# Kernel tuning notes

Hardware: AMD Instinct MI355X
Metric: run time of the kernel (lower is better)

The kernel has to match this reference:

```python
import jax, jax.numpy as jnp
import numpy as np

N_NODES = 100000
N_EDGES = 1600000
IN_CH = 128
HID = 128
OUT_CH = 64
N_GRAPHS = 512


def gcn_conv(x, edge_index, W, b):
    # GCNConv (PyG defaults): add self-loops, symmetric normalization
    # out = D^{-1/2} (A + I) D^{-1/2} X W + b
    n = x.shape[0]
    loop = jnp.arange(n, dtype=edge_index.dtype)
    src = jnp.concatenate([edge_index[0], loop])
    dst = jnp.concatenate([edge_index[1], loop])
    deg = jax.ops.segment_sum(jnp.ones_like(dst, x.dtype), dst, num_segments=n)
    dinv = jnp.where(deg > 0, jax.lax.rsqrt(deg), jnp.zeros_like(deg))
    norm = dinv[src] * dinv[dst]            # [E+N]
    h = x @ W                                # [N, out] transform first (dense GEMM)
    msg = h[src] * norm[:, None]             # gather + scale  [E+N, out]
    return jax.ops.segment_sum(msg, dst, num_segments=n) + b


def global_mean_pool(x, batch, num_graphs):
    sums = jax.ops.segment_sum(x, batch, num_segments=num_graphs)
    cnts = jax.ops.segment_sum(jnp.ones_like(batch, x.dtype), batch, num_segments=num_graphs)
    return sums / jnp.maximum(cnts, 1.0)[:, None]


def setup_inputs() -> dict:
    key = jax.random.key(0)
    ks = jax.random.split(key, 12)
    x = jax.random.normal(ks[0], (N_NODES, IN_CH), dtype=jnp.float32)
    edge_index = jax.random.randint(ks[1], (2, N_EDGES), 0, N_NODES, dtype=jnp.int64)
    batch = jnp.sort(jax.random.randint(ks[2], (N_NODES,), 0, N_GRAPHS, dtype=jnp.int64))
    def glorot(k, fi, fo):
        s = float(np.sqrt(6.0 / (fi + fo)))
        return jax.random.uniform(k, (fi, fo), jnp.float32, -s, s)
    W1 = glorot(ks[3], IN_CH, HID); b1 = jnp.zeros((HID,), jnp.float32)
    W2 = glorot(ks[4], HID, HID);   b2 = jnp.zeros((HID,), jnp.float32)
    W3 = glorot(ks[5], HID, HID);   b3 = jnp.zeros((HID,), jnp.float32)
    W4 = glorot(ks[6], HID, OUT_CH); b4 = jnp.zeros((OUT_CH,), jnp.float32)
    return {"x": x, "edge_index": edge_index, "batch": batch,
            "W1": W1, "b1": b1, "W2": W2, "b2": b2,
            "W3": W3, "b3": b3, "W4": W4, "b4": b4}


def reference(x, edge_index, batch, W1, b1, W2, b2, W3, b3, W4, b4):
    h = jax.nn.relu(gcn_conv(x, edge_index, W1, b1))
    h = jax.nn.relu(gcn_conv(h, edge_index, W2, b2))
    g = global_mean_pool(h, batch, N_GRAPHS)           # [G, HID]
    # MLP head; Dropout(0.2) is identity in eval mode
    g = jax.nn.relu(g @ W3 + b3)
    return g @ W4 + b4                                  # [G, OUT_CH]
```

## Files before the change

### kernel.cpp

```cpp
#include <hip/hip_runtime.h>

#define NN 100000
#define EE 1600000
#define CH 128
#define NG 512
#define OC 64

#define CSH 10
#define NCB 98
#define PBLK 256
#define PCHUNK 6250
#define SCAP 128

#define O_DINV   0
#define O_ROWS   200128
#define O_CNT    300160
#define O_PART   400192
#define O_OFFS   400320
#define O_CSR    400448
#define O_HS     2000448
#define O_STG    8400448
#define O_WT1    8400448
#define O_WT2    8416832
#define O_A1     14800448
#define O_START  27600448

typedef __attribute__((ext_vector_type(8))) short short8v;
typedef __attribute__((ext_vector_type(4))) float float4v;

static __device__ __forceinline__ unsigned short f2bf(float x) {
  unsigned u = __float_as_uint(x);
  return (unsigned short)((u + 0x7FFFu + ((u >> 16) & 1u)) >> 16);
}
static __device__ __forceinline__ float bf2f(unsigned short h) {
  return __uint_as_float((unsigned)h << 16);
}
static __device__ __forceinline__ float bflo(unsigned v) {
  return __uint_as_float(v << 16);
}
static __device__ __forceinline__ float bfhi(unsigned v) {
  return __uint_as_float(v & 0xFFFF0000u);
}

__global__ __launch_bounds__(1024) void k_part(const int* __restrict__ src,
                                               const int* __restrict__ dst,
                                               int* __restrict__ cnt,
                                               unsigned* __restrict__ stg) {
  __shared__ int hist[NCB];
  __shared__ int lcur[NCB];
  __shared__ unsigned lout[PCHUNK];
  int t = threadIdx.x;
  int e0 = blockIdx.x * PCHUNK;
  if (t < NCB) { hist[t] = 0; lcur[t] = 0; }
  __syncthreads();
  for (int e = e0 + t; e < e0 + PCHUNK; e += 1024)
    atomicAdd(&hist[dst[e] >> CSH], 1);
  __syncthreads();
  if (t == 0) {
    int s = 0;
    for (int i = 0; i < NCB; ++i) { int v = hist[i]; hist[i] = s; s += v; }
  }
  __syncthreads();
  for (int e = e0 + t; e < e0 + PCHUNK; e += 1024) {
    int d = dst[e];
    int b = d >> CSH;
    int p = hist[b] + atomicAdd(&lcur[b], 1);
    lout[p] = (unsigned)src[e] | ((unsigned)(d & 1023) << 17);
  }
  __syncthreads();
  int w = t >> 6, lane = t & 63;
  unsigned* mystg = stg + (size_t)blockIdx.x * NCB * SCAP;
  for (int b = w; b < NCB; b += 16) {
    int beg = hist[b];
    int end = (b == NCB - 1) ? PCHUNK : hist[b + 1];
    int n = min(end - beg, SCAP);
    for (int i = lane; i < n; i += 64) mystg[b * SCAP + i] = lout[beg + i];
    if (lane == 0) cnt[blockIdx.x * NCB + b] = n;
  }
}

__global__ __launch_bounds__(1024) void k_count(const unsigned* __restrict__ stg,
                                                const int* __restrict__ cnt,
                                                int* __restrict__ rows,
                                                int* __restrict__ part,
                                                float* __restrict__ dinv) {
  __shared__ int ldeg[1024];
  __shared__ int s[1024];
  int b = blockIdx.x;
  int t = threadIdx.x;
  int w = t >> 6, lane = t & 63;
  int gid = (b << CSH) + t;
  ldeg[t] = 0;
  __syncthreads();
  for (int blk = w; blk < PBLK; blk += 16) {
    int c = cnt[blk * NCB + b];
    const unsigned* p = stg + ((size_t)blk * NCB + b) * SCAP;
    for (int e = lane; e < c; e += 64) atomicAdd(&ldeg[p[e] >> 17], 1);
  }
  __syncthreads();
  int v = ldeg[t];
  if (gid < NN) dinv[gid] = rsqrtf((float)(v + 1));
  s[t] = v;
  __syncthreads();
  for (int off = 1; off < 1024; off <<= 1) {
    int u = (t >= off) ? s[t - off] : 0;
    __syncthreads();
    if (t >= off) s[t] += u;
    __syncthreads();
  }
  if (gid < NN) rows[gid] = s[t] - v;
  if (t == 1023) part[b] = s[t];
}

__global__ void k_scan_part(const int* __restrict__ part, int* __restrict__ offs) {
  __shared__ int s[128];
  int t = threadIdx.x;
  int v = (t < NCB) ? part[t] : 0;
  s[t] = v;
  __syncthreads();
  for (int off = 1; off < 128; off <<= 1) {
    int u = (t >= off) ? s[t - off] : 0;
    __syncthreads();
    if (t >= off) s[t] += u;
    __syncthreads();
  }
  if (t < NCB) offs[t] = s[t] - v;
}

__global__ void k_scan_add(int* __restrict__ rows, const int* __restrict__ offs,
                           const int* __restrict__ batch, int* __restrict__ start) {
  int i = blockIdx.x * 256 + threadIdx.x;
  if (i >= NN) return;
  rows[i] += offs[i >> 10];
  if (i == 0) rows[NN] = EE;
  int b = batch[i];
  int prev = (i == 0) ? -1 : batch[i - 1];
  for (int g = prev + 1; g <= b; ++g) start[g] = i;
  if (i == NN - 1)
    for (int g = b + 1; g <= NG; ++g) start[g] = NN;
}

__global__ __launch_bounds__(1024) void k_place(const unsigned* __restrict__ stg,
                                                const int* __restrict__ cnt,
                                                const int* __restrict__ rows,
                                                int* __restrict__ csr) {
  __shared__ int lrow[1024];
  __shared__ int lcur[1024];
  int b = blockIdx.x;
  int t = threadIdx.x;
  int w = t >> 6, lane = t & 63;
  int gid = (b << CSH) + t;
  lrow[t] = (gid < NN) ? rows[gid] : 0;
  lcur[t] = 0;
  __syncthreads();
  for (int blk = w; blk < PBLK; blk += 16) {
    int c = cnt[blk * NCB + b];
    const unsigned* p = stg + ((size_t)blk * NCB + b) * SCAP;
    for (int e = lane; e < c; e += 64) {
      unsigned x = p[e];
      int ld = x >> 17;
      int q = atomicAdd(&lcur[ld], 1);
      csr[lrow[ld] + q] = (int)(x & 0x1FFFFu);
    }
  }
}

__global__ void k_wsplit(const float* __restrict__ W1, const float* __restrict__ W2,
                         unsigned short* __restrict__ wt1,
                         unsigned short* __restrict__ wt2) {
  int id = blockIdx.x * 256 + threadIdx.x;
  const float* W = (id < 16384) ? W1 : W2;
  unsigned short* wt = (id < 16384) ? wt1 : wt2;
  int i = id & 16383;
  int k = i >> 7, n = i & 127;
  float w = W[i];
  unsigned short h = f2bf(w);
  unsigned short l = f2bf(w - bf2f(h));
  wt[n * 128 + k] = h;
  wt[16384 + n * 128 + k] = l;
}

__global__ __launch_bounds__(256) void k_gemm_mfma(
    const float* __restrict__ X, const unsigned short* __restrict__ wth,
    const unsigned short* __restrict__ wtl, const float* __restrict__ dinv,
    unsigned short* __restrict__ Hs) {
  __shared__ __align__(16) unsigned short sWh[64 * 136];
  __shared__ __align__(16) unsigned short sWl[64 * 136];
  __shared__ __align__(16) unsigned short sXh[128 * 40];
  __shared__ __align__(16) unsigned short sXl[128 * 40];

  const int t = threadIdx.x;
  const int w = t >> 6, lane = t & 63;
  const int quad = lane >> 4, lr = lane & 15;
  const int row0 = blockIdx.x * 128;
  const int col0 = blockIdx.y * 64;

#pragma unroll
  for (int j = 0; j < 8; ++j) {
    int id = t + j * 256;
    int n = id >> 5, kk = (id & 31) * 4;
    *(ushort4*)&sWh[n * 136 + kk] = *(const ushort4*)&wth[(col0 + n) * 128 + kk];
    *(ushort4*)&sWl[n * 136 + kk] = *(const ushort4*)&wtl[(col0 + n) * 128 + kk];
  }

  float4v acc[2][4];
#pragma unroll
  for (int mi = 0; mi < 2; ++mi)
#pragma unroll
    for (int ni = 0; ni < 4; ++ni) acc[mi][ni] = (float4v){0.f, 0.f, 0.f, 0.f};

  for (int ks = 0; ks < 4; ++ks) {
    const int k0 = ks * 32;
    if (ks) __syncthreads();
#pragma unroll
    for (int i = 0; i < 4; ++i) {
      int row = i * 32 + (t >> 3);
      int seg = t & 7;
      int gr = row0 + row;
      float4 xv = {0.f, 0.f, 0.f, 0.f};
      if (gr < NN) xv = *(const float4*)&X[(size_t)gr * CH + k0 + seg * 4];
      ushort4 h, l;
      h.x = f2bf(xv.x); l.x = f2bf(xv.x - bf2f(h.x));
      h.y = f2bf(xv.y); l.y = f2bf(xv.y - bf2f(h.y));
      h.z = f2bf(xv.z); l.z = f2bf(xv.z - bf2f(h.z));
      h.w = f2bf(xv.w); l.w = f2bf(xv.w - bf2f(h.w));
      *(ushort4*)&sXh[row * 40 + seg * 4] = h;
      *(ushort4*)&sXl[row * 40 + seg * 4] = l;
    }
    __syncthreads();

    short8v ah[2], al[2];
#pragma unroll
    for (int mi = 0; mi < 2; ++mi) {
      int r = w * 32 + mi * 16 + lr;
      ah[mi] = *(const short8v*)&sXh[r * 40 + quad * 8];
      al[mi] = *(const short8v*)&sXl[r * 40 + quad * 8];
    }
#pragma unroll
    for (int ni = 0; ni < 4; ++ni) {
      int n = ni * 16 + lr;
      short8v bh = *(const short8v*)&sWh[n * 136 + k0 + quad * 8];
      short8v bl = *(const short8v*)&sWl[n * 136 + k0 + quad * 8];
#pragma unroll
      for (int mi = 0; mi < 2; ++mi) {
        acc[mi][ni] = __builtin_amdgcn_mfma_f32_16x16x32_bf16(ah[mi], bh, acc[mi][ni], 0, 0, 0);
        acc[mi][ni] = __builtin_amdgcn_mfma_f32_16x16x32_bf16(ah[mi], bl, acc[mi][ni], 0, 0, 0);
        acc[mi][ni] = __builtin_amdgcn_mfma_f32_16x16x32_bf16(al[mi], bh, acc[mi][ni], 0, 0, 0);
      }
    }
  }

#pragma unroll
  for (int mi = 0; mi < 2; ++mi) {
#pragma unroll
    for (int r = 0; r < 4; ++r) {
      int grow = row0 + w * 32 + mi * 16 + quad * 4 + r;
      if (grow < NN) {
        float d = dinv[grow];
#pragma unroll
        for (int ni = 0; ni < 4; ++ni)
          Hs[(size_t)grow * CH + col0 + ni * 16 + lr] = f2bf(d * acc[mi][ni][r]);
      }
    }
  }
}

__global__ __launch_bounds__(256) void k_aggregate(
    const unsigned* __restrict__ H, const int* __restrict__ rows,
    const int* __restrict__ csr, const float* __restrict__ dinv,
    const float* __restrict__ bias, float* __restrict__ out) {
  int node = blockIdx.x * 4 + (threadIdx.x >> 6);
  int lane = threadIdx.x & 63;
  if (node >= NN) return;
  float bx = bias[2 * lane], by = bias[2 * lane + 1];
  unsigned sv = H[(size_t)node * 64 + lane];
  float ax = bflo(sv), ay = bfhi(sv);
  int e0 = rows[node], e1 = rows[node + 1];
  int deg = e1 - e0;
  if (deg > 0) {
    int elast = e1 - 1;
    unsigned va[8], vb[8];
#pragma unroll
    for (int k = 0; k < 8; ++k) {
      int ee = e0 + k;
      int j = csr[ee <= elast ? ee : elast];
      va[k] = H[(size_t)j * 64 + lane];
    }
    int ngroups = (deg + 7) >> 3;
    int base = e0;
    for (int g = 1; g < ngroups; ++g) {
      int nb = e0 + g * 8;
#pragma unroll
      for (int k = 0; k < 8; ++k) {
        int ee = nb + k;
        int j = csr[ee <= elast ? ee : elast];
        vb[k] = H[(size_t)j * 64 + lane];
      }
#pragma unroll
      for (int k = 0; k < 8; ++k) { ax += bflo(va[k]); ay += bfhi(va[k]); }
#pragma unroll
      for (int k = 0; k < 8; ++k) va[k] = vb[k];
      base = nb;
    }
    int rem = e1 - base;
#pragma unroll
    for (int k = 0; k < 8; ++k) {
      unsigned v = (k < rem) ? va[k] : 0u;
      ax += bflo(v);
      ay += bfhi(v);
    }
  }
  float d = dinv[node];
  float2 o;
  o.x = fmaxf(fmaf(d, ax, bx), 0.f);
  o.y = fmaxf(fmaf(d, ay, by), 0.f);
  ((float2*)out)[(size_t)node * 64 + lane] = o;
}

__global__ __launch_bounds__(256) void k_head(
    const float* __restrict__ A, const int* __restrict__ start,
    const float* __restrict__ W3, const float* __restrict__ b3,
    const float* __restrict__ W4, const float* __restrict__ b4,
    float* __restrict__ out) {
  __shared__ float pooled[128];
  __shared__ float part[128];
  __shared__ float g1[128];
  int g = blockIdx.x;
  int c = threadIdx.x & 127;
  int half = threadIdx.x >> 7;
  int s0 = start[g], s1 = start[g + 1];
  float sum = 0.f;
  for (int i = s0 + half; i < s1; i += 2)
    sum += A[(size_t)i * CH + c];
  if (half) part[c] = sum;
  __syncthreads();
  if (!half) {
    float n = fmaxf((float)(s1 - s0), 1.0f);
    pooled[c] = (sum + part[c]) / n;
  }
  __syncthreads();
  if (threadIdx.x < 128) {
    float acc = b3[c];
    for (int k = 0; k < 128; ++k) acc += pooled[k] * W3[k * CH + c];
    g1[c] = fmaxf(acc, 0.f);
  }
  __syncthreads();
  if (threadIdx.x < 64) {
    float acc = b4[threadIdx.x];
    for (int k = 0; k < 128; ++k) acc += g1[k] * W4[k * OC + threadIdx.x];
    out[(size_t)g * OC + threadIdx.x] = acc;
  }
}

extern "C" void kernel_launch(void* const* d_in, const int* in_sizes, int n_in,
                              void* d_out, int out_size, void* d_ws, size_t ws_size,
                              hipStream_t stream) {
  const float* X   = (const float*)d_in[0];
  const int* ei    = (const int*)d_in[1];
  const int* batch = (const int*)d_in[2];
  const float* W1  = (const float*)d_in[3];
  const float* b1  = (const float*)d_in[4];
  const float* W2  = (const float*)d_in[5];
  const float* b2  = (const float*)d_in[6];
  const float* W3  = (const float*)d_in[7];
  const float* b3  = (const float*)d_in[8];
  const float* W4  = (const float*)d_in[9];
  const float* b4  = (const float*)d_in[10];
  float* out = (float*)d_out;
  float* ws = (float*)d_ws;

  const int* src = ei;
  const int* dst = ei + EE;

  float* dinv = ws + O_DINV;
  int* rows   = (int*)(ws + O_ROWS);
  int* cnt    = (int*)(ws + O_CNT);
  int* part   = (int*)(ws + O_PART);
  int* offs   = (int*)(ws + O_OFFS);
  int* csr    = (int*)(ws + O_CSR);
  unsigned short* Hs = (unsigned short*)(ws + O_HS);
  unsigned* stg = (unsigned*)(ws + O_STG);
  unsigned short* wt1 = (unsigned short*)(ws + O_WT1);
  unsigned short* wt2 = (unsigned short*)(ws + O_WT2);
  float* A1   = ws + O_A1;
  int* start  = (int*)(ws + O_START);

  k_part<<<PBLK, 1024, 0, stream>>>(src, dst, cnt, stg);
  k_count<<<NCB, 1024, 0, stream>>>(stg, cnt, rows, part, dinv);
  k_scan_part<<<1, 128, 0, stream>>>(part, offs);
  k_scan_add<<<(NN + 255) / 256, 256, 0, stream>>>(rows, offs, batch, start);
  k_place<<<NCB, 1024, 0, stream>>>(stg, cnt, rows, csr);
  k_wsplit<<<128, 256, 0, stream>>>(W1, W2, wt1, wt2);

  dim3 ggrid((NN + 127) / 128, 2);
  k_gemm_mfma<<<ggrid, 256, 0, stream>>>(X, wt1, wt1 + 16384, dinv, Hs);
  k_aggregate<<<(NN + 3) / 4, 256, 0, stream>>>((const unsigned*)Hs, rows, csr, dinv, b1, A1);
  k_gemm_mfma<<<ggrid, 256, 0, stream>>>(A1, wt2, wt2 + 16384, dinv, Hs);
  k_aggregate<<<(NN + 3) / 4, 256, 0, stream>>>((const unsigned*)Hs, rows, csr, dinv, b2, A1);

  k_head<<<NG, 256, 0, stream>>>(A1, start, W3, b3, W4, b4, out);
}
```

Baseline: 404.1 us.

## Pad CSR rows to multiples of eight with zero-row sentinel to drop tail masking

Each node's CSR row length is rounded up to a multiple of 8 and the padding slots point to a sentinel row NN, whose H entry is zeroed by the GEMM kernel. The aggregation loop then reads full groups of 8 with no clamping or remainder masking, and uses 32-bit index arithmetic. The trade-off is about 3.5 extra padded gathers per node, all hitting the same cached zero row, plus a repacked workspace layout.

```diff
diff --git a/kernel.cpp b/kernel.cpp
--- a/kernel.cpp
+++ b/kernel.cpp
@@ -13,17 +13,17 @@
 #define SCAP 128
 
 #define O_DINV   0
-#define O_ROWS   200128
-#define O_CNT    300160
-#define O_PART   400192
-#define O_OFFS   400320
-#define O_CSR    400448
-#define O_HS     2000448
-#define O_STG    8400448
-#define O_WT1    8400448
-#define O_WT2    8416832
+#define O_ROWS   100032
+#define O_CNT    200064
+#define O_PART   225152
+#define O_OFFS   225280
+#define O_START  225408
+#define O_CSR    225984
+#define O_HS     2726016
+#define O_STG    9126080
+#define O_WT1    9126080
+#define O_WT2    9142464
 #define O_A1     14800448
-#define O_START  27600448
 
 typedef __attribute__((ext_vector_type(8))) short short8v;
 typedef __attribute__((ext_vector_type(4))) float float4v;
@@ -100,7 +100,8 @@
   __syncthreads();
   int v = ldeg[t];
   if (gid < NN) dinv[gid] = rsqrtf((float)(v + 1));
-  s[t] = v;
+  int pdeg = (v + 7) & ~7;
+  s[t] = pdeg;
   __syncthreads();
   for (int off = 1; off < 1024; off <<= 1) {
     int u = (t >= off) ? s[t - off] : 0;
@@ -108,7 +109,7 @@
     if (t >= off) s[t] += u;
     __syncthreads();
   }
-  if (gid < NN) rows[gid] = s[t] - v;
+  if (gid < NN) rows[gid] = s[t] - pdeg;
   if (t == 1023) part[b] = s[t];
 }
 
@@ -128,11 +129,12 @@
 }
 
 __global__ void k_scan_add(int* __restrict__ rows, const int* __restrict__ offs,
+                           const int* __restrict__ part,
                            const int* __restrict__ batch, int* __restrict__ start) {
   int i = blockIdx.x * 256 + threadIdx.x;
   if (i >= NN) return;
   rows[i] += offs[i >> 10];
-  if (i == 0) rows[NN] = EE;
+  if (i == 0) rows[NN] = offs[NCB - 1] + part[NCB - 1];
   int b = batch[i];
   int prev = (i == 0) ? -1 : batch[i - 1];
   for (int g = prev + 1; g <= b; ++g) start[g] = i;
@@ -163,6 +165,11 @@
       csr[lrow[ld] + q] = (int)(x & 0x1FFFFu);
     }
   }
+  __syncthreads();
+  int d = lcur[t];
+  int pd = (d + 7) & ~7;
+  int base = lrow[t];
+  for (int i = d; i < pd; ++i) csr[base + i] = NN;
 }
 
 __global__ void k_wsplit(const float* __restrict__ W1, const float* __restrict__ W2,
@@ -195,6 +202,9 @@
   const int row0 = blockIdx.x * 128;
   const int col0 = blockIdx.y * 64;
 
+  if (blockIdx.x == 0 && blockIdx.y == 0 && t < 64)
+    *(unsigned*)&Hs[(size_t)NN * CH + t * 2] = 0u;
+
 #pragma unroll
   for (int j = 0; j < 8; ++j) {
     int id = t + j * 256;
@@ -273,42 +283,25 @@
   int lane = threadIdx.x & 63;
   if (node >= NN) return;
   float bx = bias[2 * lane], by = bias[2 * lane + 1];
-  unsigned sv = H[(size_t)node * 64 + lane];
+  unsigned sv = H[((unsigned)node << 6) | lane];
   float ax = bflo(sv), ay = bfhi(sv);
   int e0 = rows[node], e1 = rows[node + 1];
-  int deg = e1 - e0;
-  if (deg > 0) {
-    int elast = e1 - 1;
+  if (e1 > e0) {
     unsigned va[8], vb[8];
 #pragma unroll
-    for (int k = 0; k < 8; ++k) {
-      int ee = e0 + k;
-      int j = csr[ee <= elast ? ee : elast];
-      va[k] = H[(size_t)j * 64 + lane];
-    }
-    int ngroups = (deg + 7) >> 3;
-    int base = e0;
-    for (int g = 1; g < ngroups; ++g) {
-      int nb = e0 + g * 8;
-#pragma unroll
-      for (int k = 0; k < 8; ++k) {
-        int ee = nb + k;
-        int j = csr[ee <= elast ? ee : elast];
-        vb[k] = H[(size_t)j * 64 + lane];
-      }
+    for (int k = 0; k < 8; ++k)
+      va[k] = H[((unsigned)csr[e0 + k] << 6) | lane];
+    for (int base = e0 + 8; base < e1; base += 8) {
+#pragma unroll
+      for (int k = 0; k < 8; ++k)
+        vb[k] = H[((unsigned)csr[base + k] << 6) | lane];
 #pragma unroll
       for (int k = 0; k < 8; ++k) { ax += bflo(va[k]); ay += bfhi(va[k]); }
 #pragma unroll
       for (int k = 0; k < 8; ++k) va[k] = vb[k];
-      base = nb;
-    }
-    int rem = e1 - base;
-#pragma unroll
-    for (int k = 0; k < 8; ++k) {
-      unsigned v = (k < rem) ? va[k] : 0u;
-      ax += bflo(v);
-      ay += bfhi(v);
-    }
+    }
+#pragma unroll
+    for (int k = 0; k < 8; ++k) { ax += bflo(va[k]); ay += bfhi(va[k]); }
   }
   float d = dinv[node];
   float2 o;
@@ -377,18 +370,18 @@
   int* cnt    = (int*)(ws + O_CNT);
   int* part   = (int*)(ws + O_PART);
   int* offs   = (int*)(ws + O_OFFS);
+  int* start  = (int*)(ws + O_START);
   int* csr    = (int*)(ws + O_CSR);
   unsigned short* Hs = (unsigned short*)(ws + O_HS);
   unsigned* stg = (unsigned*)(ws + O_STG);
   unsigned short* wt1 = (unsigned short*)(ws + O_WT1);
   unsigned short* wt2 = (unsigned short*)(ws + O_WT2);
   float* A1   = ws + O_A1;
-  int* start  = (int*)(ws + O_START);
 
   k_part<<<PBLK, 1024, 0, stream>>>(src, dst, cnt, stg);
   k_count<<<NCB, 1024, 0, stream>>>(stg, cnt, rows, part, dinv);
   k_scan_part<<<1, 128, 0, stream>>>(part, offs);
-  k_scan_add<<<(NN + 255) / 256, 256, 0, stream>>>(rows, offs, batch, start);
+  k_scan_add<<<(NN + 255) / 256, 256, 0, stream>>>(rows, offs, part, batch, start);
   k_place<<<NCB, 1024, 0, stream>>>(stg, cnt, rows, csr);
   k_wsplit<<<128, 256, 0, stream>>>(W1, W2, wt1, wt2);
 
```

Measured after the change: 404.9 us (median of 2 runs). About the same (+0.2%).
